# Kernel tuning notes

Measured on AMD Instinct MI355X. Metric: run time of the kernel, lower is better.

Reference implementation:

```python
import jax, jax.numpy as jnp
import numpy as np

N_NODES = 50000
N_EDGES = 800000
DIM = 64


def _param(key, shape, scale):
    return jax.random.normal(key, shape, dtype=jnp.float32) * scale


def setup_inputs() -> dict:
    key = jax.random.key(0)
    ks = jax.random.split(key, 20)
    s = 1.0 / np.sqrt(DIM)
    x = jax.random.normal(ks[0], (N_NODES, DIM), dtype=jnp.float32)
    weights = jax.random.uniform(ks[1], (6,), dtype=jnp.float32)
    edge_index = jax.random.randint(ks[2], (2, N_EDGES), 0, N_NODES, dtype=jnp.int64)
    return {
        "x": x,
        "weights": weights,
        # mlp
        "W_mlp": _param(ks[3], (DIM, DIM), s), "b_mlp": jnp.zeros((DIM,), jnp.float32),
        # sage (mean aggregator): lin_l on neighbor mean, lin_r on self
        "Wl_sage": _param(ks[4], (DIM, DIM), s), "Wr_sage": _param(ks[5], (DIM, DIM), s),
        "b_sage": jnp.zeros((DIM,), jnp.float32),
        # gcn
        "W_gcn": _param(ks[6], (DIM, DIM), s), "b_gcn": jnp.zeros((DIM,), jnp.float32),
        # gat (single head)
        "W_gat": _param(ks[7], (DIM, DIM), s),
        "a_src": _param(ks[8], (DIM,), s), "a_dst": _param(ks[9], (DIM,), s),
        "b_gat": jnp.zeros((DIM,), jnp.float32),
        # chebconv K=3
        "W_cheb": _param(ks[10], (3, DIM, DIM), s), "b_cheb": jnp.zeros((DIM,), jnp.float32),
        # gin (eps=0, nn = Linear)
        "W_gin": _param(ks[11], (DIM, DIM), s), "b_gin": jnp.zeros((DIM,), jnp.float32),
        "edge_index": edge_index,
    }


def _mixed_forward(x, weights, W_mlp, b_mlp, Wl_sage, Wr_sage, b_sage,
                   W_gcn, b_gcn, W_gat, a_src, a_dst, b_gat,
                   W_cheb, b_cheb, W_gin, b_gin, edge_index):
    N = x.shape[0]
    src, dst = edge_index[0], edge_index[1]
    seg_sum = lambda v, idx: jax.ops.segment_sum(v, idx, num_segments=N)

    deg = seg_sum(jnp.ones(src.shape[0], x.dtype), dst)  # in-degree [N]
    nsum = seg_sum(x[src], dst)                           # sum of neighbor feats [N, D]

    # --- mlp (graph-free) ---
    o_mlp = x @ W_mlp + b_mlp

    # --- sage, mean aggregation ---
    nmean = nsum / jnp.maximum(deg, 1.0)[:, None]
    o_sage = nmean @ Wl_sage + x @ Wr_sage + b_sage

    # --- gcn with self loops: D'^{-1/2} (A+I) D'^{-1/2} X W ---
    dinv = jax.lax.rsqrt(deg + 1.0)
    xw = x @ W_gcn
    norm_e = dinv[src] * dinv[dst]
    o_gcn = seg_sum(norm_e[:, None] * xw[src], dst) + xw * (dinv * dinv)[:, None] + b_gcn

    # --- gat, single head, self loops appended, leaky_relu(0.2) scoring ---
    h = x @ W_gat
    el, er = h @ a_src, h @ a_dst
    loop = jnp.arange(N, dtype=src.dtype)
    src2 = jnp.concatenate([src, loop])
    dst2 = jnp.concatenate([dst, loop])
    e = jax.nn.leaky_relu(el[src2] + er[dst2], 0.2)
    m = jax.ops.segment_max(e, dst2, num_segments=N)
    p = jnp.exp(e - m[dst2])
    z = jax.ops.segment_sum(p, dst2, num_segments=N)
    alpha = p / (z[dst2] + 1e-16)
    o_gat = jax.ops.segment_sum(alpha[:, None] * h[src2], dst2, num_segments=N) + b_gat

    # --- cheb K=3, lambda_max=2: L_hat = L_norm - I = -A_norm ---
    dinv_c = jax.lax.rsqrt(jnp.maximum(deg, 1.0))
    nrm = dinv_c[src] * dinv_c[dst]
    prop = lambda t: seg_sum(nrm[:, None] * t[src], dst)
    T0 = x
    T1 = -prop(T0)
    T2 = -2.0 * prop(T1) - T0
    o_cheb = T0 @ W_cheb[0] + T1 @ W_cheb[1] + T2 @ W_cheb[2] + b_cheb

    # --- gin, eps=0, nn = Linear ---
    o_gin = (x + nsum) @ W_gin + b_gin

    outs = (o_mlp, o_sage, o_gcn, o_gat, o_cheb, o_gin)
    res = jnp.zeros_like(o_mlp)
    for k, o in enumerate(outs):
        res = res + weights[k] * jax.nn.elu(o)
    return res


def reference(x, weights, W_mlp, b_mlp, Wl_sage, Wr_sage, b_sage,
              W_gcn, b_gcn, W_gat, a_src, a_dst, b_gat,
              W_cheb, b_cheb, W_gin, b_gin, edge_index):
    return _mixed_forward(x, weights, W_mlp, b_mlp, Wl_sage, Wr_sage, b_sage,
                          W_gcn, b_gcn, W_gat, a_src, a_dst, b_gat,
                          W_cheb, b_cheb, W_gin, b_gin, edge_index)
```

## Files before the change

kernel.cpp:

```cpp
#include <hip/hip_runtime.h>
#include <cstdint>
#include <cstddef>

#define NN 50000
#define NE 800000
#define CAP 96
#define NSEG 8
#define SEGW 6250

constexpr size_t O_CNT   = 0;
constexpr size_t O_SLOT  = 50048;
constexpr size_t O_NODAL = O_SLOT + (size_t)NN*CAP;
constexpr size_t O_VA    = O_NODAL + 200000;
constexpr size_t O_VB    = O_VA + 64;
constexpr size_t O_XB    = O_VB + 64;
constexpr size_t O_NSB   = O_XB + 1600032;
constexpr size_t O_T1B   = O_NSB + 1600000;
constexpr size_t O_V1B   = O_T1B + 1600032;
constexpr size_t O_GB    = O_V1B + 1600000;
constexpr size_t O_UB    = O_GB  + 1600000;
constexpr size_t O_WPK   = O_UB  + 1600000;

typedef __attribute__((ext_vector_type(8))) short short8;
typedef __attribute__((ext_vector_type(4))) float f32x4;

__device__ __forceinline__ float leaky02(float v){ return v >= 0.f ? v : 0.2f*v; }
__device__ __forceinline__ float eluf(float v){ return v > 0.f ? v : (__expf(v) - 1.f); }

__device__ __forceinline__ void lds_fence(){
  asm volatile("s_waitcnt lgkmcnt(0)" ::: "memory");
}

__device__ __forceinline__ unsigned short f2bf(float f){
  unsigned u = __float_as_uint(f);
  unsigned r = (u + 0x7FFFu + ((u >> 16) & 1u)) >> 16;
  return (unsigned short)r;
}
__device__ __forceinline__ float bf2f(unsigned short b){
  return __uint_as_float(((unsigned)b) << 16);
}
__device__ __forceinline__ unsigned pack2(unsigned short lo, unsigned short hi){
  return (unsigned)lo | ((unsigned)hi << 16);
}

__global__ __launch_bounds__(256) void k_scatter(
    const int* __restrict__ src, const int* __restrict__ dst,
    int* __restrict__ cnt, unsigned short* __restrict__ slot,
    const float* __restrict__ W_mlp, const float* __restrict__ Wr,
    const float* __restrict__ W_cheb, const float* __restrict__ W_gin,
    const float* __restrict__ Wl, const float* __restrict__ W_gcn,
    const float* __restrict__ W_gat,
    const float* __restrict__ a_src, const float* __restrict__ a_dst,
    const float4* __restrict__ x4,
    float* __restrict__ va, float* __restrict__ vb,
    unsigned short* __restrict__ wpk,
    ushort4* __restrict__ xb4, ushort4* __restrict__ t1b4){
  int b = blockIdx.x;
  int seg = b & (NSEG-1);
  int lo = seg * SEGW;
  int e = (b >> 3)*256 + threadIdx.x;
  if (e < NE){
    int d = dst[e];
    if ((unsigned)(d - lo) < (unsigned)SEGW){
      int s = src[e];
      int pos = atomicAdd(&cnt[d], 1);
      if (pos < CAP) slot[(size_t)d*CAP + pos] = (unsigned short)s;
    }
  }
  if (b == 0){
    int k = threadIdx.x;
    if (k < 64){
      float sa = 0.f, sb = 0.f;
      for (int j = 0; j < 64; ++j){
        float w = W_gat[k*64 + j];
        sa = fmaf(w, a_src[j], sa);
        sb = fmaf(w, a_dst[j], sb);
      }
      va[k] = sa; vb[k] = sb;
    }
  } else if (b <= 9){
    int w = b - 1;
    const float* s; const float* sub = nullptr;
    switch (w){
      case 0: s = W_mlp; break;
      case 1: s = Wr; break;
      case 2: s = W_cheb; sub = W_cheb + 8192; break;
      case 3: s = W_gin; break;
      case 4: s = Wl; break;
      case 5: s = W_cheb + 4096; break;
      case 6: s = W_cheb + 8192; break;
      case 7: s = W_gcn; break;
      default: s = W_gat; break;
    }
    for (int ee = threadIdx.x; ee < 4096; ee += 256){
      int k = ee >> 6, n = ee & 63;
      float f = s[ee];
      if (sub) f -= sub[ee];
      wpk[(size_t)w*4096 + (size_t)n*64 + k] = f2bf(f);
    }
  } else if (b < 3136){
    int i = (b - 10)*256 + threadIdx.x;
    if (i < NN*16){
      float4 v = x4[i];
      ushort4 o;
      o.x = f2bf(v.x); o.y = f2bf(v.y); o.z = f2bf(v.z); o.w = f2bf(v.w);
      xb4[i] = o;
    } else if (i < (NN+1)*16){
      ushort4 z; z.x = 0; z.y = 0; z.z = 0; z.w = 0;
      xb4[i] = z;
      t1b4[i] = z;
    }
  }
}

__global__ __launch_bounds__(256) void k_nodal(const unsigned short* __restrict__ xb,
    const int* __restrict__ cnt, const float* __restrict__ va, const float* __restrict__ vb,
    float4* __restrict__ nodal){
  int tid = threadIdx.x;
  int li = tid & 15;
  int row = blockIdx.x*16 + (tid >> 4);
  if (row >= NN) return;
  ushort4 hb = *(const ushort4*)&xb[(size_t)row*64 + li*4];
  float4 hv = make_float4(bf2f(hb.x), bf2f(hb.y), bf2f(hb.z), bf2f(hb.w));
  float4 av = *(const float4*)&va[li*4];
  float4 bv = *(const float4*)&vb[li*4];
  float ps = hv.x*av.x + hv.y*av.y + hv.z*av.z + hv.w*av.w;
  float pd = hv.x*bv.x + hv.y*bv.y + hv.z*bv.z + hv.w*bv.w;
  #pragma unroll
  for (int o = 1; o < 16; o <<= 1){ ps += __shfl_xor(ps, o); pd += __shfl_xor(pd, o); }
  if (li == 0){
    float c = (float)cnt[row];
    float dinv  = rsqrtf(c + 1.f);
    float dinvc = rsqrtf(fmaxf(c, 1.f));
    nodal[row] = make_float4(dinvc, dinv, ps, pd);
  }
}

__global__ __launch_bounds__(256) void k_aggA(
    const unsigned short* __restrict__ xb,
    const int* __restrict__ cnt, const unsigned short* __restrict__ slot,
    const float4* __restrict__ nodal,
    unsigned* __restrict__ nsb2, unsigned* __restrict__ t1b2,
    unsigned* __restrict__ v1b2, unsigned* __restrict__ gb2){
  __shared__ float4 sW[4][64];
  int wid  = threadIdx.x >> 6;
  int lane = threadIdx.x & 63;
  int half = lane >> 5, hl = lane & 31;
  int b    = blockIdx.x;
  int seg  = b & (NSEG-1);
  int idx  = b >> 3;
  int lbase = idx*8 + wid*2 + half;
  bool vld = lbase < SEGW;
  int node = seg*SEGW + (vld ? lbase : 0);
  int c = vld ? min(cnt[node], CAP) : 0;
  int cmax = max(c, __shfl_xor(c, 32));
  const unsigned short* sl = slot + (size_t)node*CAP;
  float4 nn = nodal[node];
  float ern = nn.w;
  float a0e=0.f,a0o=0.f,a1e=0.f,a1o=0.f,a2e=0.f,a2o=0.f,a3e=0.f,a3o=0.f, zl=0.f;
  for (int base = 0; base < cmax; base += 32){
    int rem = c - base;
    bool act = hl < rem;
    int s = act ? (int)sl[base+hl] : NN;
    float4 ns = act ? nodal[s] : make_float4(0.f,0.f,0.f,0.f);
    float p = act ? __expf(fminf(leaky02(ns.z + ern), 60.f)) : 0.f;
    zl += p;
    sW[wid][lane] = make_float4(__int_as_float(s), ns.x, ns.y, p);
    lds_fence();
    int remw = min(32, cmax - base);
    for (int j = 0; j < remw; j += 8){
      float4 w[8]; unsigned uv[8];
      #pragma unroll
      for (int q2 = 0; q2 < 8; ++q2){
        w[q2] = sW[wid][half*32 + j + q2];
        int sb = __float_as_int(w[q2].x);
        sb = ((unsigned)sb <= (unsigned)NN) ? sb : NN;
        uv[q2] = *(const unsigned*)&xb[(size_t)sb*64 + 2*hl];
      }
      #pragma unroll
      for (int q2 = 0; q2 < 8; ++q2){
        float lo = __uint_as_float(uv[q2] << 16);
        float hi = __uint_as_float(uv[q2] & 0xffff0000u);
        a0e += lo;                       a0o += hi;
        a1e = fmaf(w[q2].y, lo, a1e);    a1o = fmaf(w[q2].y, hi, a1o);
        a2e = fmaf(w[q2].z, lo, a2e);    a2o = fmaf(w[q2].z, hi, a2o);
        a3e = fmaf(w[q2].w, lo, a3e);    a3o = fmaf(w[q2].w, hi, a3o);
      }
    }
    lds_fence();
  }
  #pragma unroll
  for (int o = 1; o <= 16; o <<= 1) zl += __shfl_xor(zl, o);
  unsigned uxs = *(const unsigned*)&xb[(size_t)node*64 + 2*hl];
  float xsx = __uint_as_float(uxs << 16);
  float xsy = __uint_as_float(uxs & 0xffff0000u);
  float p_self = __expf(fminf(leaky02(nn.z + nn.w), 60.f));
  float rz = 1.f / (zl + p_self + 1e-16f);
  if (vld){
    size_t off2 = (size_t)node*32 + hl;
    nsb2[off2] = pack2(f2bf(a0e), f2bf(a0o));
    t1b2[off2] = pack2(f2bf(-nn.x*a1e), f2bf(-nn.x*a1o));
    v1b2[off2] = pack2(f2bf(nn.y*a2e + nn.y*nn.y*xsx), f2bf(nn.y*a2o + nn.y*nn.y*xsy));
    gb2[off2]  = pack2(f2bf((a3e + p_self*xsx)*rz), f2bf((a3o + p_self*xsy)*rz));
  }
}

__global__ __launch_bounds__(256) void k_aggB(const unsigned short* __restrict__ t1b,
    const int* __restrict__ cnt, const unsigned short* __restrict__ slot,
    const float4* __restrict__ nodal, unsigned* __restrict__ ub2){
  __shared__ float2 sW[4][64];
  int wid  = threadIdx.x >> 6;
  int lane = threadIdx.x & 63;
  int half = lane >> 5, hl = lane & 31;
  int b    = blockIdx.x;
  int seg  = b & (NSEG-1);
  int idx  = b >> 3;
  int lbase = idx*8 + wid*2 + half;
  bool vld = lbase < SEGW;
  int node = seg*SEGW + (vld ? lbase : 0);
  int c = vld ? min(cnt[node], CAP) : 0;
  int cmax = max(c, __shfl_xor(c, 32));
  const unsigned short* sl = slot + (size_t)node*CAP;
  const float* nf = (const float*)nodal;
  float ae = 0.f, ao = 0.f;
  for (int base = 0; base < cmax; base += 32){
    int rem = c - base;
    bool act = hl < rem;
    int s = act ? (int)sl[base+hl] : NN;
    float dc = act ? nf[(size_t)s*4] : 0.f;
    sW[wid][lane] = make_float2(__int_as_float(s), dc);
    lds_fence();
    int remw = min(32, cmax - base);
    for (int j = 0; j < remw; j += 8){
      float2 w[8]; unsigned uv[8];
      #pragma unroll
      for (int q2 = 0; q2 < 8; ++q2){
        w[q2] = sW[wid][half*32 + j + q2];
        int sb = __float_as_int(w[q2].x);
        sb = ((unsigned)sb <= (unsigned)NN) ? sb : NN;
        uv[q2] = *(const unsigned*)&t1b[(size_t)sb*64 + 2*hl];
      }
      #pragma unroll
      for (int q2 = 0; q2 < 8; ++q2){
        float lo = __uint_as_float(uv[q2] << 16);
        float hi = __uint_as_float(uv[q2] & 0xffff0000u);
        ae = fmaf(w[q2].y, lo, ae);
        ao = fmaf(w[q2].y, hi, ao);
      }
    }
    lds_fence();
  }
  if (vld){
    float sc = -2.f * nodal[node].x;
    ub2[(size_t)node*32 + hl] = pack2(f2bf(sc*ae), f2bf(sc*ao));
  }
}

__global__ __launch_bounds__(64) void k_epi3(
    const float* __restrict__ wts,
    const float* __restrict__ b_mlp, const float* __restrict__ b_sage,
    const float* __restrict__ b_gcn, const float* __restrict__ b_gat,
    const float* __restrict__ b_cheb, const float* __restrict__ b_gin,
    const float4* __restrict__ nodal, const unsigned short* __restrict__ wpk,
    const unsigned short* __restrict__ xb, const unsigned short* __restrict__ nsb,
    const unsigned short* __restrict__ t1b, const unsigned short* __restrict__ v1b,
    const unsigned short* __restrict__ gb, const unsigned short* __restrict__ ub,
    float* __restrict__ out){
  const int lane = threadIdx.x;
  const int ml   = lane & 15;
  const int q    = lane >> 4;
  const int b    = blockIdx.x;
  const int seg  = b & (NSEG-1);
  const int idx  = b >> 3;
  const int rowbase = seg*SEGW + idx*16;
  const int nvalid  = min(16, SEGW - idx*16);

  const int ar = (ml < nvalid) ? (rowbase + ml) : NN;
  const size_t ro = (size_t)ar*64 + q*8;
  short8 Au0  = *(const short8*)(ub  + ro), Au1  = *(const short8*)(ub  + ro + 32);
  short8 Av10 = *(const short8*)(v1b + ro), Av11 = *(const short8*)(v1b + ro + 32);
  short8 Ag0  = *(const short8*)(gb  + ro), Ag1  = *(const short8*)(gb  + ro + 32);
  short8 At0  = *(const short8*)(t1b + ro), At1  = *(const short8*)(t1b + ro + 32);
  short8 Ax0  = *(const short8*)(xb  + ro), Ax1  = *(const short8*)(xb  + ro + 32);
  short8 An0  = *(const short8*)(nsb + ro), An1  = *(const short8*)(nsb + ro + 32);

  const float w0 = wts[0], w1 = wts[1], w2 = wts[2], w3 = wts[3], w4 = wts[4], w5 = wts[5];
  const float* nod = (const float*)nodal;

  auto group = [&](int w, const short8& a0, const short8& a1, f32x4 acc[4]){
    const unsigned short* base = wpk + (size_t)w*4096;
    #pragma unroll
    for (int nt = 0; nt < 4; ++nt){
      const unsigned short* bp = base + (size_t)(nt*16 + ml)*64;
      short8 b0 = *(const short8*)(bp + q*8);
      short8 b1 = *(const short8*)(bp + 32 + q*8);
      acc[nt] = __builtin_amdgcn_mfma_f32_16x16x32_bf16(a0, b0, acc[nt], 0, 0, 0);
      acc[nt] = __builtin_amdgcn_mfma_f32_16x16x32_bf16(a1, b1, acc[nt], 0, 0, 0);
    }
  };

  f32x4 res[4];
  #pragma unroll
  for (int i = 0; i < 4; ++i) res[i] = (f32x4){0.f,0.f,0.f,0.f};

  auto emit = [&](const f32x4 acc[4], const float* __restrict__ bias, float wk){
    #pragma unroll
    for (int nt = 0; nt < 4; ++nt){
      float bsv = bias[nt*16 + ml];
      #pragma unroll
      for (int r = 0; r < 4; ++r) res[nt][r] += wk * eluf(acc[nt][r] + bsv);
    }
  };

  f32x4 t[4], accC[4], accWr[4], accG[4];

  #pragma unroll
  for (int i=0;i<4;++i) accC[i] = (f32x4){0.f,0.f,0.f,0.f};
  group(6, Au0, Au1, accC);
  group(5, At0, At1, accC);
  #pragma unroll
  for (int i=0;i<4;++i) t[i] = (f32x4){0.f,0.f,0.f,0.f};
  group(7, Av10, Av11, t); emit(t, b_gcn, w2);
  #pragma unroll
  for (int i=0;i<4;++i) t[i] = (f32x4){0.f,0.f,0.f,0.f};
  group(8, Ag0, Ag1, t); emit(t, b_gat, w3);
  #pragma unroll
  for (int i=0;i<4;++i) t[i] = (f32x4){0.f,0.f,0.f,0.f};
  group(0, Ax0, Ax1, t); emit(t, b_mlp, w0);
  #pragma unroll
  for (int i=0;i<4;++i) accWr[i] = (f32x4){0.f,0.f,0.f,0.f};
  group(1, Ax0, Ax1, accWr);
  group(2, Ax0, Ax1, accC); emit(accC, b_cheb, w4);
  #pragma unroll
  for (int i=0;i<4;++i) accG[i] = (f32x4){0.f,0.f,0.f,0.f};
  group(3, Ax0, Ax1, accG);
  group(3, An0, An1, accG); emit(accG, b_gin, w5);
  #pragma unroll
  for (int i=0;i<4;++i) t[i] = (f32x4){0.f,0.f,0.f,0.f};
  group(4, An0, An1, t);
  #pragma unroll
  for (int nt = 0; nt < 4; ++nt){
    float bsv = b_sage[nt*16 + ml];
    #pragma unroll
    for (int r = 0; r < 4; ++r){
      int lr = q*4 + r;
      int row = rowbase + lr;
      if (lr < nvalid){
        float dc = nod[(size_t)row*4];
        float invd = dc*dc;
        res[nt][r] += w1 * eluf(invd*t[nt][r] + accWr[nt][r] + bsv);
      }
    }
  }
  #pragma unroll
  for (int nt = 0; nt < 4; ++nt){
    int col = nt*16 + ml;
    #pragma unroll
    for (int r = 0; r < 4; ++r){
      int lr = q*4 + r;
      if (lr < nvalid){
        int row = rowbase + lr;
        out[(size_t)row*64 + col] = res[nt][r];
      }
    }
  }
}

extern "C" void kernel_launch(void* const* d_in, const int* in_sizes, int n_in,
                              void* d_out, int out_size, void* d_ws, size_t ws_size,
                              hipStream_t stream){
  const float* x      = (const float*)d_in[0];
  const float* wts    = (const float*)d_in[1];
  const float* W_mlp  = (const float*)d_in[2];
  const float* b_mlp  = (const float*)d_in[3];
  const float* Wl     = (const float*)d_in[4];
  const float* Wr     = (const float*)d_in[5];
  const float* b_sage = (const float*)d_in[6];
  const float* W_gcn  = (const float*)d_in[7];
  const float* b_gcn  = (const float*)d_in[8];
  const float* W_gat  = (const float*)d_in[9];
  const float* a_src  = (const float*)d_in[10];
  const float* a_dst  = (const float*)d_in[11];
  const float* b_gat  = (const float*)d_in[12];
  const float* W_cheb = (const float*)d_in[13];
  const float* b_cheb = (const float*)d_in[14];
  const float* W_gin  = (const float*)d_in[15];
  const float* b_gin  = (const float*)d_in[16];
  const int*   ei     = (const int*)d_in[17];

  float* wsf  = (float*)d_ws;
  int*  cnt   = (int*)d_ws;
  unsigned short* slot = (unsigned short*)(wsf + O_SLOT);
  float4* nodal = (float4*)(wsf + O_NODAL);
  float* va   = wsf + O_VA;
  float* vb   = wsf + O_VB;
  unsigned short* xbu = (unsigned short*)(wsf + O_XB);
  unsigned short* nsb = (unsigned short*)(wsf + O_NSB);
  unsigned short* t1b = (unsigned short*)(wsf + O_T1B);
  unsigned short* v1b = (unsigned short*)(wsf + O_V1B);
  unsigned short* gb  = (unsigned short*)(wsf + O_GB);
  unsigned short* ub  = (unsigned short*)(wsf + O_UB);
  unsigned short* wpk = (unsigned short*)(wsf + O_WPK);
  float* out  = (float*)d_out;

  hipMemsetAsync(cnt, 0, NN*sizeof(int), stream);
  k_scatter <<<25000,256, 0, stream>>>(ei, ei + NE, cnt, slot,
                                       W_mlp, Wr, W_cheb, W_gin, Wl, W_gcn, W_gat,
                                       a_src, a_dst, (const float4*)x,
                                       va, vb, wpk, (ushort4*)xbu, (ushort4*)t1b);
  k_nodal   <<<3125, 256, 0, stream>>>(xbu, cnt, va, vb, nodal);
  k_aggA    <<<6256, 256, 0, stream>>>(xbu, cnt, slot, nodal,
                                       (unsigned*)nsb, (unsigned*)t1b,
                                       (unsigned*)v1b, (unsigned*)gb);
  k_aggB    <<<6256, 256, 0, stream>>>(t1b, cnt, slot, nodal, (unsigned*)ub);
  k_epi3    <<<3128,  64, 0, stream>>>(wts, b_mlp, b_sage, b_gcn, b_gat, b_cheb, b_gin,
                                       nodal, wpk, xbu, nsb, t1b, v1b, gb, ub, out);
}
```

Baseline: 221.2 us.

## Stage packed weights in swizzled LDS, shared across four waves per block

The epilogue kernel now runs four wavefronts per block over 64 rows instead of one wavefront over 16. Each 64x64 bf16 weight group is cooperatively loaded into double-buffered XOR-swizzled shared memory and reused by all four waves. This replaces per-wave global/L2 weight reads. The cost is a barrier after every group stage and fewer, larger blocks (784), which lowers parallelism granularity for a small kernel.

After: 202.3 us, median of 2. 8.6% less time.

```diff
diff --git a/kernel.cpp b/kernel.cpp
--- a/kernel.cpp
+++ b/kernel.cpp
@@ -7,6 +7,7 @@
 #define CAP 96
 #define NSEG 8
 #define SEGW 6250
+#define EPB 64
 
 constexpr size_t O_CNT   = 0;
 constexpr size_t O_SLOT  = 50048;
@@ -256,7 +257,7 @@
   }
 }
 
-__global__ __launch_bounds__(64) void k_epi3(
+__global__ __launch_bounds__(256) void k_epi4(
     const float* __restrict__ wts,
     const float* __restrict__ b_mlp, const float* __restrict__ b_sage,
     const float* __restrict__ b_gcn, const float* __restrict__ b_gat,
@@ -266,14 +267,17 @@
     const unsigned short* __restrict__ t1b, const unsigned short* __restrict__ v1b,
     const unsigned short* __restrict__ gb, const unsigned short* __restrict__ ub,
     float* __restrict__ out){
-  const int lane = threadIdx.x;
+  __shared__ unsigned short lb[2][4096];
+  const int tid  = threadIdx.x;
+  const int wid  = tid >> 6;
+  const int lane = tid & 63;
   const int ml   = lane & 15;
   const int q    = lane >> 4;
   const int b    = blockIdx.x;
   const int seg  = b & (NSEG-1);
   const int idx  = b >> 3;
-  const int rowbase = seg*SEGW + idx*16;
-  const int nvalid  = min(16, SEGW - idx*16);
+  const int rowbase = seg*SEGW + idx*EPB + wid*16;
+  const int nvalid  = min(16, max(0, SEGW - idx*EPB - wid*16));
 
   const int ar = (ml < nvalid) ? (rowbase + ml) : NN;
   const size_t ro = (size_t)ar*64 + q*8;
@@ -287,13 +291,25 @@
   const float w0 = wts[0], w1 = wts[1], w2 = wts[2], w3 = wts[3], w4 = wts[4], w5 = wts[5];
   const float* nod = (const float*)nodal;
 
-  auto group = [&](int w, const short8& a0, const short8& a1, f32x4 acc[4]){
-    const unsigned short* base = wpk + (size_t)w*4096;
+  auto stage = [&](int g, int s){
+    const unsigned short* gp = wpk + (size_t)g*4096;
+    int u0 = tid*16;
+    short8 v0 = *(const short8*)(gp + u0);
+    short8 v1 = *(const short8*)(gp + u0 + 8);
+    int row = u0 >> 6;
+    int sw  = (row & 7) << 3;
+    int w0i = u0 & 63;
+    *(short8*)&lb[s][row*64 + (w0i ^ sw)]       = v0;
+    *(short8*)&lb[s][row*64 + ((w0i + 8) ^ sw)] = v1;
+  };
+  auto groupL = [&](int s, const short8& a0, const short8& a1, f32x4 acc[4]){
     #pragma unroll
     for (int nt = 0; nt < 4; ++nt){
-      const unsigned short* bp = base + (size_t)(nt*16 + ml)*64;
-      short8 b0 = *(const short8*)(bp + q*8);
-      short8 b1 = *(const short8*)(bp + 32 + q*8);
+      int r  = nt*16 + ml;
+      int sw = (r & 7) << 3;
+      const unsigned short* bp = &lb[s][r*64];
+      short8 b0 = *(const short8*)(bp + ((q*8) ^ sw));
+      short8 b1 = *(const short8*)(bp + ((32 + q*8) ^ sw));
       acc[nt] = __builtin_amdgcn_mfma_f32_16x16x32_bf16(a0, b0, acc[nt], 0, 0, 0);
       acc[nt] = __builtin_amdgcn_mfma_f32_16x16x32_bf16(a1, b1, acc[nt], 0, 0, 0);
     }
@@ -302,7 +318,6 @@
   f32x4 res[4];
   #pragma unroll
   for (int i = 0; i < 4; ++i) res[i] = (f32x4){0.f,0.f,0.f,0.f};
-
   auto emit = [&](const f32x4 acc[4], const float* __restrict__ bias, float wk){
     #pragma unroll
     for (int nt = 0; nt < 4; ++nt){
@@ -313,39 +328,45 @@
   };
 
   f32x4 t[4], accC[4], accWr[4], accG[4];
-
-  #pragma unroll
-  for (int i=0;i<4;++i) accC[i] = (f32x4){0.f,0.f,0.f,0.f};
-  group(6, Au0, Au1, accC);
-  group(5, At0, At1, accC);
-  #pragma unroll
-  for (int i=0;i<4;++i) t[i] = (f32x4){0.f,0.f,0.f,0.f};
-  group(7, Av10, Av11, t); emit(t, b_gcn, w2);
-  #pragma unroll
-  for (int i=0;i<4;++i) t[i] = (f32x4){0.f,0.f,0.f,0.f};
-  group(8, Ag0, Ag1, t); emit(t, b_gat, w3);
-  #pragma unroll
-  for (int i=0;i<4;++i) t[i] = (f32x4){0.f,0.f,0.f,0.f};
-  group(0, Ax0, Ax1, t); emit(t, b_mlp, w0);
-  #pragma unroll
-  for (int i=0;i<4;++i) accWr[i] = (f32x4){0.f,0.f,0.f,0.f};
-  group(1, Ax0, Ax1, accWr);
-  group(2, Ax0, Ax1, accC); emit(accC, b_cheb, w4);
-  #pragma unroll
-  for (int i=0;i<4;++i) accG[i] = (f32x4){0.f,0.f,0.f,0.f};
-  group(3, Ax0, Ax1, accG);
-  group(3, An0, An1, accG); emit(accG, b_gin, w5);
-  #pragma unroll
-  for (int i=0;i<4;++i) t[i] = (f32x4){0.f,0.f,0.f,0.f};
-  group(4, An0, An1, t);
+  #pragma unroll
+  for (int i=0;i<4;++i){ accC[i]=(f32x4){0.f,0.f,0.f,0.f}; }
+
+  stage(6, 0); __syncthreads();
+  groupL(0, Au0,  Au1,  accC); stage(5, 1); __syncthreads();
+  groupL(1, At0,  At1,  accC); stage(7, 0); __syncthreads();
+  #pragma unroll
+  for (int i=0;i<4;++i) t[i]=(f32x4){0.f,0.f,0.f,0.f};
+  groupL(0, Av10, Av11, t);    stage(8, 1); __syncthreads();
+  emit(t, b_gcn, w2);
+  #pragma unroll
+  for (int i=0;i<4;++i) t[i]=(f32x4){0.f,0.f,0.f,0.f};
+  groupL(1, Ag0,  Ag1,  t);    stage(0, 0); __syncthreads();
+  emit(t, b_gat, w3);
+  #pragma unroll
+  for (int i=0;i<4;++i) t[i]=(f32x4){0.f,0.f,0.f,0.f};
+  groupL(0, Ax0,  Ax1,  t);    stage(1, 1); __syncthreads();
+  emit(t, b_mlp, w0);
+  #pragma unroll
+  for (int i=0;i<4;++i) accWr[i]=(f32x4){0.f,0.f,0.f,0.f};
+  groupL(1, Ax0,  Ax1,  accWr); stage(2, 0); __syncthreads();
+  groupL(0, Ax0,  Ax1,  accC);  stage(3, 1); __syncthreads();
+  emit(accC, b_cheb, w4);
+  #pragma unroll
+  for (int i=0;i<4;++i) accG[i]=(f32x4){0.f,0.f,0.f,0.f};
+  groupL(1, Ax0,  Ax1,  accG);  stage(3, 0); __syncthreads();
+  groupL(0, An0,  An1,  accG);  stage(4, 1); __syncthreads();
+  emit(accG, b_gin, w5);
+  #pragma unroll
+  for (int i=0;i<4;++i) t[i]=(f32x4){0.f,0.f,0.f,0.f};
+  groupL(1, An0,  An1,  t);
   #pragma unroll
   for (int nt = 0; nt < 4; ++nt){
     float bsv = b_sage[nt*16 + ml];
     #pragma unroll
     for (int r = 0; r < 4; ++r){
       int lr = q*4 + r;
-      int row = rowbase + lr;
       if (lr < nvalid){
+        int row = rowbase + lr;
         float dc = nod[(size_t)row*4];
         float invd = dc*dc;
         res[nt][r] += w1 * eluf(invd*t[nt][r] + accWr[nt][r] + bsv);
@@ -413,6 +434,6 @@
                                        (unsigned*)nsb, (unsigned*)t1b,
                                        (unsigned*)v1b, (unsigned*)gb);
   k_aggB    <<<6256, 256, 0, stream>>>(t1b, cnt, slot, nodal, (unsigned*)ub);
-  k_epi3    <<<3128,  64, 0, stream>>>(wts, b_mlp, b_sage, b_gcn, b_gat, b_cheb, b_gin,
+  k_epi4    <<<784,  256, 0, stream>>>(wts, b_mlp, b_sage, b_gcn, b_gat, b_cheb, b_gin,
                                        nodal, wpk, xbu, nsb, t1b, v1b, gb, ub, out);
 }
```
